# Kernel optimization log

Hardware: AMD Instinct MI355X
Metric: run time of the kernel (lower is better)

## Reference

```python
import jax, jax.numpy as jnp
import numpy as np

HIDDEN = 1024
FFN = 3584
NUM_EXPERTS = 8
TOP_K = 2
B, S = 2, 1024


def setup_inputs() -> dict:
    key = jax.random.key(0)
    k0, k1, k2, k3 = jax.random.split(key, 4)
    hidden_states = jax.random.normal(k0, (B, S, HIDDEN), dtype=jnp.float32)
    # torch Linear stores [out, in]; we keep gate as [E, H] (matches nn.Linear weight)
    gate_w = jax.random.normal(k1, (NUM_EXPERTS, HIDDEN), dtype=jnp.float32) * 0.02
    # GroupedLinear weights stored as [E, in, out] for direct x @ W per expert
    w_gate_up = jax.random.normal(k2, (NUM_EXPERTS, HIDDEN, 2 * FFN), dtype=jnp.float32) * 0.02
    w_down = jax.random.normal(k3, (NUM_EXPERTS, FFN, HIDDEN), dtype=jnp.float32) * 0.02
    return {"hidden_states": hidden_states, "gate_w": gate_w,
            "w_gate_up": w_gate_up, "w_down": w_down}


def reference(hidden_states, gate_w, w_gate_up, w_down):
    b, s, h = hidden_states.shape
    x = hidden_states.reshape(-1, h)                      # [T, H]
    T = x.shape[0]
    E = gate_w.shape[0]

    # Router: logits -> fp32 softmax -> top-k -> renormalize (Mixtral semantics)
    router_logits = x @ gate_w.T                          # [T, E]
    probs = jax.nn.softmax(router_logits.astype(jnp.float32), axis=-1)
    top_vals, top_idx = jax.lax.top_k(probs, TOP_K)       # [T, K]
    top_vals = top_vals / top_vals.sum(axis=-1, keepdims=True)
    top_vals = top_vals.astype(x.dtype)

    # Dense combine weights [T, E]: scatter top-k probs to expert slots.
    # Equivalent to permute -> grouped GEMM -> unpermute-with-probs.
    combine = jnp.zeros((T, E), dtype=x.dtype).at[
        jnp.arange(T)[:, None], top_idx].add(top_vals)

    out = jnp.zeros_like(x)
    for e in range(E):  # fixed small expert count
        gu = x @ w_gate_up[e]                             # [T, 2F]
        gate_proj, up_proj = jnp.split(gu, 2, axis=-1)
        act = jax.nn.silu(gate_proj) * up_proj            # [T, F]
        out = out + combine[:, e:e + 1] * (act @ w_down[e])

    return out.reshape(b, s, h), router_logits
```

## Files before the change

kernel.cpp:

```cpp
#include <hip/hip_runtime.h>
#include <hip/hip_bf16.h>
#include <stdint.h>

#define HIDDEN  1024
#define FFN     3584
#define NE      8
#define NTOK    2048
#define CAP     2048
#define OUT_ELEMS (NTOK * HIDDEN)

#define X_OFF    0u
#define CNT_OFF  (4u*1024u*1024u)
#define TOK_OFF  (CNT_OFF + 256u)
#define WGT_OFF  (TOK_OFF + 65536u)
#define INV_OFF  (WGT_OFF + 65536u)
#define ACT_OFF  (INV_OFF + 16384u)
#define ACT_SZ   (4096u * 3584u * 2u)
#define WGU_OFF  (ACT_OFF + ACT_SZ)
#define WGU_SZ   (8u*56u*16u*16384u)
#define WDB_OFF  (WGU_OFF + WGU_SZ)
#define WDB_SZ   (8u*8u*56u*16384u)
#define PART_OFF (WDB_OFF + WDB_SZ)
#define PART_SZ  (4096u*1024u*4u)
#define WS_NEED  ((size_t)PART_OFF + (size_t)PART_SZ)

typedef __attribute__((ext_vector_type(8))) short short8;
typedef __attribute__((ext_vector_type(4))) float floatx4;

static __device__ __forceinline__ uint32_t f2bf(float f) {
  union { float f; uint32_t u; } v; v.f = f;
  return (v.u + 0x7FFFu + ((v.u >> 16) & 1u)) >> 16;
}
static __device__ __forceinline__ uint32_t pack2(float lo, float hi) {
  return f2bf(lo) | (f2bf(hi) << 16);
}
union S8U { uint4 u; short8 s; };
static __device__ __forceinline__ short8 as_short8(uint4 v) { S8U x; x.u = v; return x.s; }

static __device__ __forceinline__ void ld_g2l16(const void* g, void* l) {
  __builtin_amdgcn_global_load_lds(
      (const __attribute__((address_space(1))) void*)g,
      (__attribute__((address_space(3))) void*)l, 16, 0, 0);
}

static __device__ __forceinline__ void stage_tile(
    const char* const* aptr, const char* bptr, size_t akt, size_t bkt,
    uint4* AsB, uint4* BsB, int w)
{
#pragma unroll
  for (int it = 0; it < 4; ++it)
    ld_g2l16(aptr[it] + akt, &AsB[(w * 4 + it) * 64]);
#pragma unroll
  for (int it = 0; it < 4; ++it)
    ld_g2l16(bptr + bkt + (size_t)it * 1024u, &BsB[(w * 4 + it) * 64]);
}

#define WAIT_VM8()  do { __builtin_amdgcn_sched_barrier(0); \
                         asm volatile("s_waitcnt vmcnt(8)" ::: "memory"); \
                         __builtin_amdgcn_sched_barrier(0); } while (0)
#define WAIT_VM16() do { __builtin_amdgcn_sched_barrier(0); \
                         asm volatile("s_waitcnt vmcnt(16)" ::: "memory"); \
                         __builtin_amdgcn_sched_barrier(0); } while (0)
#define WAIT_VM0()  do { __builtin_amdgcn_sched_barrier(0); \
                         asm volatile("s_waitcnt vmcnt(0)" ::: "memory"); \
                         __builtin_amdgcn_sched_barrier(0); } while (0)
#define WAIT_LGKM() do { asm volatile("s_waitcnt lgkmcnt(0)" ::: "memory"); } while (0)
#define BAR()       do { __builtin_amdgcn_s_barrier(); \
                         __builtin_amdgcn_sched_barrier(0); } while (0)
#define ENDBAR()    do { __builtin_amdgcn_sched_barrier(0); \
                         __builtin_amdgcn_s_barrier(); } while (0)

__global__ __launch_bounds__(256) void moe_prep(float4* __restrict__ out4,
                                                int* __restrict__ cnt) {
  uint32_t i = blockIdx.x * 256u + threadIdx.x;
  out4[i] = make_float4(0.f, 0.f, 0.f, 0.f);
  if (blockIdx.x == 0 && threadIdx.x < NE) cnt[threadIdx.x] = 0;
}

__global__ __launch_bounds__(256) void moe_convert(const float4* __restrict__ x4,
                                                   uint4* __restrict__ xb,
                                                   int* __restrict__ cnt) {
  uint32_t g = blockIdx.x * 256u + threadIdx.x;
  float4 a = x4[2u*g], b = x4[2u*g + 1u];
  xb[g] = make_uint4(pack2(a.x, a.y), pack2(a.z, a.w),
                     pack2(b.x, b.y), pack2(b.z, b.w));
  if (blockIdx.x == 0 && threadIdx.x < NE) cnt[threadIdx.x] = 0;
}

__global__ __launch_bounds__(256) void moe_router(
    const float* __restrict__ x, const float* __restrict__ gw,
    float* __restrict__ logits, int* __restrict__ cnt,
    int* __restrict__ tok, float* __restrict__ wgt, int* __restrict__ inv)
{
  const int t = blockIdx.x * 4 + (threadIdx.x >> 6);
  const int lane = threadIdx.x & 63;
  const float* xr = x + (size_t)t * HIDDEN;
  float a[NE];
#pragma unroll
  for (int e = 0; e < NE; ++e) a[e] = 0.f;
  for (int hh = 0; hh < HIDDEN / 64; ++hh) {
    float xv = xr[hh * 64 + lane];
#pragma unroll
    for (int e = 0; e < NE; ++e) a[e] += xv * gw[e * HIDDEN + hh * 64 + lane];
  }
#pragma unroll
  for (int off = 32; off > 0; off >>= 1) {
#pragma unroll
    for (int e = 0; e < NE; ++e) a[e] += __shfl_xor(a[e], off);
  }
  if (lane == 0) {
#pragma unroll
    for (int e = 0; e < NE; ++e) logits[t * NE + e] = a[e];
    int i0 = 0; float v0 = a[0];
#pragma unroll
    for (int e = 1; e < NE; ++e) if (a[e] > v0) { v0 = a[e]; i0 = e; }
    int i1 = (i0 == 0) ? 1 : 0; float v1 = a[i1];
#pragma unroll
    for (int e = 0; e < NE; ++e) if (e != i0 && a[e] > v1) { v1 = a[e]; i1 = e; }
    float w0 = 1.f / (1.f + __expf(v1 - v0));
    float w1 = 1.f - w0;
    int p0 = atomicAdd(&cnt[i0], 1); tok[i0 * CAP + p0] = t; wgt[i0 * CAP + p0] = w0;
    int p1 = atomicAdd(&cnt[i1], 1); tok[i1 * CAP + p1] = t; wgt[i1 * CAP + p1] = w1;
    inv[t * 2 + 0] = i0 * CAP + p0;
    inv[t * 2 + 1] = i1 * CAP + p1;
  }
}

__global__ __launch_bounds__(256) void moe_wconv_d(const float* __restrict__ wd,
                                                   uint4* __restrict__ wdb) {
  const int kt = blockIdx.x, nb = blockIdx.y, e = blockIdx.z;
  const int n0 = nb * 128, k0 = kt * 64;
  const float* wB = wd + (size_t)e * FFN * HIDDEN;
  uint4* dst = wdb + ((size_t)(e * 8 + nb) * 56 + kt) * 1024;

  __shared__ float lds_f[64 * 129];

#pragma unroll
  for (int p = 0; p < 8; ++p) {
    int idx = p * 256 + threadIdx.x;
    int r   = idx >> 5;
    int lc  = (idx & 31) * 4;
    float4 v = *(const float4*)(wB + (size_t)(k0 + r) * HIDDEN + n0 + lc);
    float* d = &lds_f[r * 129 + lc];
    d[0] = v.x; d[1] = v.y; d[2] = v.z; d[3] = v.w;
  }
  __syncthreads();
#pragma unroll
  for (int p = 0; p < 4; ++p) {
    int m  = p * 256 + threadIdx.x;
    int ne = m >> 3, c8 = m & 7;
    float f[8];
#pragma unroll
    for (int kk = 0; kk < 8; ++kk) f[kk] = lds_f[(c8 * 8 + kk) * 129 + ne];
    dst[ne * 8 + (c8 ^ (ne & 7))] =
        make_uint4(pack2(f[0], f[1]), pack2(f[2], f[3]),
                   pack2(f[4], f[5]), pack2(f[6], f[7]));
  }
}

__global__ __launch_bounds__(512) void moe_gateup_f(
    const uint4* __restrict__ xb, const float* __restrict__ wgu,
    const int* __restrict__ cnt, const int* __restrict__ tok,
    unsigned short* __restrict__ act)
{
  const int e  = blockIdx.z;
  const int m0 = blockIdx.y * 512;
  const int fb = blockIdx.x;
  const int f0 = fb * 64;
  const int cn = cnt[e];
  if (m0 >= cn) return;
  int basev = 0;
#pragma unroll
  for (int i = 0; i < NE; ++i) { int ci = cnt[i]; if (i < e) basev += ci; }

  __shared__ uint4 As[4096];
  __shared__ uint4 Bs[1024];

  const int tid  = threadIdx.x;
  const int lane = tid & 63;
  const int w    = tid >> 6;
  const int q    = lane >> 4;
  const int c    = lane & 15;

  const int* tokE = tok + e * CAP;
  const char* aptr[8];
#pragma unroll
  for (int it = 0; it < 8; ++it) {
    int p   = (w * 8 + it) * 64 + lane;
    int row = p >> 3, c8 = p & 7;
    int mrow = m0 + row; if (mrow >= cn) mrow = cn - 1;
    aptr[it] = (const char*)(xb + (size_t)tokE[mrow] * (HIDDEN / 8) + (c8 ^ (row & 7)));
  }

  const int ne  = tid & 127;
  const int c8b = tid >> 7;
  const int col = f0 + ((ne >> 6) << 5) + (ne & 31) + (((ne >> 5) & 1) ? FFN : 0);
  const float* colp = wgu + (size_t)e * HIDDEN * (2 * FFN) + col;
  const int wi0 = ne * 8 + (c8b ^ (ne & 7));
  const int wi1 = ne * 8 + ((c8b + 4) ^ (ne & 7));

  floatx4 acc[4][8];
#pragma unroll
  for (int i = 0; i < 4; ++i)
#pragma unroll
    for (int j = 0; j < 8; ++j) acc[i][j] = (floatx4){0.f, 0.f, 0.f, 0.f};

  float rv[16];
#pragma unroll
  for (int s = 0; s < 2; ++s)
#pragma unroll
    for (int kk = 0; kk < 8; ++kk)
      rv[s * 8 + kk] = colp[(size_t)((c8b + 4 * s) * 8 + kk) * (2 * FFN)];

  const int NT = HIDDEN / 64;
  for (int kt = 0; kt < NT; ++kt) {
    WAIT_VM0();
    uint4 pk0 = make_uint4(pack2(rv[0], rv[1]),  pack2(rv[2], rv[3]),
                           pack2(rv[4], rv[5]),  pack2(rv[6], rv[7]));
    uint4 pk1 = make_uint4(pack2(rv[8], rv[9]),  pack2(rv[10], rv[11]),
                           pack2(rv[12], rv[13]), pack2(rv[14], rv[15]));
    Bs[wi0] = pk0;
    Bs[wi1] = pk1;
#pragma unroll
    for (int it = 0; it < 8; ++it)
      ld_g2l16(aptr[it] + (size_t)kt * 128u, &As[(w * 8 + it) * 64]);
    if (kt + 1 < NT) {
      const int kb = (kt + 1) * 64;
#pragma unroll
      for (int s = 0; s < 2; ++s)
#pragma unroll
        for (int kk = 0; kk < 8; ++kk)
          rv[s * 8 + kk] = colp[(size_t)(kb + (c8b + 4 * s) * 8 + kk) * (2 * FFN)];
      WAIT_VM16();
    } else {
      WAIT_VM0();
    }
    WAIT_LGKM();
    BAR();
#pragma unroll
    for (int ks = 0; ks < 2; ++ks) {
      const int kc8 = ks * 4 + q;
      short8 af[4];
#pragma unroll
      for (int i = 0; i < 4; ++i) {
        int row = w * 64 + i * 16 + c;
        af[i] = as_short8(As[row * 8 + (kc8 ^ (row & 7))]);
      }
      short8 bfr[8];
#pragma unroll
      for (int j = 0; j < 8; ++j) {
        int n = j * 16 + c;
        bfr[j] = as_short8(Bs[n * 8 + (kc8 ^ (n & 7))]);
      }
#pragma unroll
      for (int i = 0; i < 4; ++i)
#pragma unroll
        for (int j = 0; j < 8; ++j)
          acc[i][j] = __builtin_amdgcn_mfma_f32_16x16x32_bf16(af[i], bfr[j], acc[i][j], 0, 0, 0);
    }
    ENDBAR();
  }

#pragma unroll
  for (int i = 0; i < 4; ++i) {
#pragma unroll
    for (int r = 0; r < 4; ++r) {
      int m = m0 + w * 64 + i * 16 + q * 4 + r;
      if (m < cn) {
        unsigned short* arow = act + (size_t)(basev + m) * FFN;
#pragma unroll
        for (int t4 = 0; t4 < 4; ++t4) {
          const int jj = (t4 & 1) | ((t4 >> 1) << 2);
          float g = acc[i][jj][r];
          float u = acc[i][jj + 2][r];
          float a = (g / (1.f + __expf(-g))) * u;
          arow[f0 + ((jj >> 2) << 5) + (jj & 1) * 16 + c] = (unsigned short)f2bf(a);
        }
      }
    }
  }
}

__global__ __launch_bounds__(256) void moe_down(
    const unsigned short* __restrict__ act, const uint4* __restrict__ wdb,
    const int* __restrict__ cnt, const int* __restrict__ tok,
    const float* __restrict__ wgt, float* __restrict__ part)
{
  const int e  = blockIdx.z;
  const int m0 = blockIdx.y * 128;
  const int nb = blockIdx.x;
  const int n0 = nb * 128;
  const int cn = cnt[e];
  if (m0 >= cn) return;
  int basev = 0;
#pragma unroll
  for (int i = 0; i < NE; ++i) { int ci = cnt[i]; if (i < e) basev += ci; }

  __shared__ uint4 As[2][1024];
  __shared__ uint4 Bs4[2][1024];

  const int tid  = threadIdx.x;
  const int lane = tid & 63;
  const int w    = tid >> 6;
  const int wm   = w >> 1, wn = w & 1;
  const int q    = lane >> 4;
  const int c    = lane & 15;

  const char* aptr[4];
#pragma unroll
  for (int it = 0; it < 4; ++it) {
    int p   = (w * 4 + it) * 64 + lane;
    int row = p >> 3, c8 = p & 7;
    int mrow = m0 + row; if (mrow >= cn) mrow = cn - 1;
    aptr[it] = (const char*)act +
               ((size_t)(basev + mrow) * FFN + (size_t)((c8 ^ (row & 7)) * 8)) * 2u;
  }
  const char* bptr = (const char*)wdb + ((size_t)(e * 8 + nb) * 56) * 16384u
                   + (size_t)w * 4096u + (size_t)lane * 16u;

  floatx4 acc[4][4];
#pragma unroll
  for (int i = 0; i < 4; ++i)
#pragma unroll
    for (int j = 0; j < 4; ++j) acc[i][j] = (floatx4){0.f, 0.f, 0.f, 0.f};

  const int NT = FFN / 64;
  stage_tile(aptr, bptr, 0, 0, As[0], Bs4[0], w);
  int cur = 0;
  for (int kt = 0; kt < NT; ++kt) {
    if (kt + 1 < NT) {
      stage_tile(aptr, bptr, (size_t)(kt + 1) * 128u, (size_t)(kt + 1) * 16384u,
                 As[cur ^ 1], Bs4[cur ^ 1], w);
      WAIT_VM8();
    } else {
      WAIT_VM0();
    }
    BAR();
    const uint4* Asc = As[cur];
    const uint4* Bsc = Bs4[cur];
#pragma unroll
    for (int ks = 0; ks < 2; ++ks) {
      const int kc8 = ks * 4 + q;
      short8 af[4];
#pragma unroll
      for (int i = 0; i < 4; ++i) {
        int row = wm * 64 + i * 16 + c;
        af[i] = as_short8(Asc[row * 8 + (kc8 ^ (row & 7))]);
      }
      short8 bfr[4];
#pragma unroll
      for (int j = 0; j < 4; ++j) {
        int n = wn * 64 + j * 16 + c;
        bfr[j] = as_short8(Bsc[n * 8 + (kc8 ^ (n & 7))]);
      }
#pragma unroll
      for (int i = 0; i < 4; ++i)
#pragma unroll
        for (int j = 0; j < 4; ++j)
          acc[i][j] = __builtin_amdgcn_mfma_f32_16x16x32_bf16(af[i], bfr[j], acc[i][j], 0, 0, 0);
    }
    ENDBAR();
    cur ^= 1;
  }

#pragma unroll
  for (int i = 0; i < 4; ++i) {
#pragma unroll
    for (int r = 0; r < 4; ++r) {
      int m = m0 + wm * 64 + i * 16 + q * 4 + r;
      if (m < cn) {
        float  wg   = wgt[e * CAP + m];
        float* prow = part + (size_t)(basev + m) * HIDDEN + n0 + wn * 64 + c;
#pragma unroll
        for (int j = 0; j < 4; ++j)
          prow[j * 16] = acc[i][j][r] * wg;
      }
    }
  }
}

__global__ __launch_bounds__(256) void moe_combine(
    const int* __restrict__ cnt, const int* __restrict__ inv,
    const float4* __restrict__ part4, float4* __restrict__ out4)
{
  const int t  = blockIdx.x;
  const int s0 = inv[2 * t], s1 = inv[2 * t + 1];
  const int e0 = s0 >> 11, e1 = s1 >> 11;
  int b0 = 0, b1 = 0;
#pragma unroll
  for (int i = 0; i < NE; ++i) {
    int ci = cnt[i];
    if (i < e0) b0 += ci;
    if (i < e1) b1 += ci;
  }
  const size_t r0 = (size_t)(b0 + (s0 & (CAP - 1))) * 256u;
  const size_t r1 = (size_t)(b1 + (s1 & (CAP - 1))) * 256u;
  const int i = threadIdx.x;
  float4 a = part4[r0 + i];
  float4 b = part4[r1 + i];
  out4[(size_t)t * 256u + i] = make_float4(a.x + b.x, a.y + b.y, a.z + b.z, a.w + b.w);
}

__global__ __launch_bounds__(256) void moe_gateup_lg(
    const uint4* __restrict__ xb, const float* __restrict__ wgu,
    const int* __restrict__ cnt, const int* __restrict__ tok,
    unsigned short* __restrict__ act)
{
  const int e  = blockIdx.z;
  const int m0 = blockIdx.y * 128;
  const int f0 = blockIdx.x * 64;
  const int cn = cnt[e];
  if (m0 >= cn) return;
  int basev = 0;
#pragma unroll
  for (int i = 0; i < NE; ++i) { int ci = cnt[i]; if (i < e) basev += ci; }

  __shared__ uint4    As[1024];
  __shared__ uint32_t Bs[4096];

  const int tid  = threadIdx.x;
  const int lane = tid & 63;
  const int w    = tid >> 6;
  const int wm   = w >> 1, wn = w & 1;
  const int q    = lane >> 4;
  const int c    = lane & 15;

  floatx4 acc[4][4];
#pragma unroll
  for (int i = 0; i < 4; ++i)
#pragma unroll
    for (int j = 0; j < 4; ++j) acc[i][j] = (floatx4){0.f, 0.f, 0.f, 0.f};

  const float* wB  = wgu + (size_t)e * HIDDEN * (2 * FFN);
  const int* tokE  = tok + e * CAP;

  for (int kt = 0; kt < HIDDEN / 64; ++kt) {
    const int k0 = kt * 64;
    __syncthreads();
#pragma unroll
    for (int it = 0; it < 4; ++it) {
      int cid = it * 256 + tid;
      int row = cid >> 3, c8 = cid & 7;
      int mrow = m0 + row; if (mrow >= cn) mrow = cn - 1;
      int tk = tokE[mrow];
      As[row * 8 + (c8 ^ (row & 7))] = xb[(size_t)tk * (HIDDEN / 8) + (k0 >> 3) + c8];
    }
#pragma unroll
    for (int it = 0; it < 4; ++it) {
      int mid = it * 256 + tid;
      int kp = mid >> 5;
      int n  = (mid & 31) * 4;
      int col = f0 + ((n >> 6) << 5) + (n & 31) + (((n >> 5) & 1) ? FFN : 0);
      const float* src = wB + (size_t)(k0 + 2 * kp) * (2 * FFN) + col;
      float4 r0 = *(const float4*)src;
      float4 r1 = *(const float4*)(src + 2 * FFN);
      int widx = kp * 128 + (n ^ (((kp >> 2) & 1) << 4));
      *(uint4*)&Bs[widx] = make_uint4(pack2(r0.x, r1.x), pack2(r0.y, r1.y),
                                      pack2(r0.z, r1.z), pack2(r0.w, r1.w));
    }
    __syncthreads();
#pragma unroll
    for (int ks = 0; ks < 2; ++ks) {
      short8 af[4];
#pragma unroll
      for (int i = 0; i < 4; ++i) {
        int row = wm * 64 + i * 16 + c;
        int kc8 = ks * 4 + q;
        af[i] = as_short8(As[row * 8 + (kc8 ^ (row & 7))]);
      }
      short8 bfr[4];
#pragma unroll
      for (int j = 0; j < 4; ++j) {
        int n  = wn * 64 + j * 16 + c;
        int kp = ks * 16 + q * 4;
        int nn = n ^ ((q & 1) << 4);
        bfr[j] = as_short8(make_uint4(Bs[(kp + 0) * 128 + nn], Bs[(kp + 1) * 128 + nn],
                                      Bs[(kp + 2) * 128 + nn], Bs[(kp + 3) * 128 + nn]));
      }
#pragma unroll
      for (int i = 0; i < 4; ++i)
#pragma unroll
        for (int j = 0; j < 4; ++j)
          acc[i][j] = __builtin_amdgcn_mfma_f32_16x16x32_bf16(af[i], bfr[j], acc[i][j], 0, 0, 0);
    }
  }

#pragma unroll
  for (int i = 0; i < 4; ++i) {
#pragma unroll
    for (int r = 0; r < 4; ++r) {
      int m = m0 + wm * 64 + i * 16 + q * 4 + r;
      if (m < cn) {
#pragma unroll
        for (int j = 0; j < 2; ++j) {
          float g = acc[i][j][r];
          float u = acc[i][j + 2][r];
          float a = (g / (1.f + __expf(-g))) * u;
          act[(size_t)(basev + m) * FFN + (f0 + wn * 32 + j * 16 + c)] = (unsigned short)f2bf(a);
        }
      }
    }
  }
}

__global__ __launch_bounds__(256) void moe_down_lg(
    const uint4* __restrict__ actc, const float* __restrict__ wd,
    const int* __restrict__ cnt, const int* __restrict__ tok,
    const float* __restrict__ wgt, float* __restrict__ out)
{
  const int e  = blockIdx.z;
  const int m0 = blockIdx.y * 128;
  const int n0 = blockIdx.x * 128;
  const int cn = cnt[e];
  if (m0 >= cn) return;
  int basev = 0;
#pragma unroll
  for (int i = 0; i < NE; ++i) { int ci = cnt[i]; if (i < e) basev += ci; }

  __shared__ uint4    As[1024];
  __shared__ uint32_t Bs[4096];

  const int tid  = threadIdx.x;
  const int lane = tid & 63;
  const int w    = tid >> 6;
  const int wm   = w >> 1, wn = w & 1;
  const int q    = lane >> 4;
  const int c    = lane & 15;

  floatx4 acc[4][4];
#pragma unroll
  for (int i = 0; i < 4; ++i)
#pragma unroll
    for (int j = 0; j < 4; ++j) acc[i][j] = (floatx4){0.f, 0.f, 0.f, 0.f};

  const float* wB = wd + (size_t)e * FFN * HIDDEN;

  for (int kt = 0; kt < FFN / 64; ++kt) {
    const int k0 = kt * 64;
    __syncthreads();
#pragma unroll
    for (int it = 0; it < 4; ++it) {
      int cid = it * 256 + tid;
      int row = cid >> 3, c8 = cid & 7;
      int mrow = m0 + row; if (mrow >= cn) mrow = cn - 1;
      As[row * 8 + (c8 ^ (row & 7))] =
          actc[(size_t)(basev + mrow) * (FFN / 8) + (k0 >> 3) + c8];
    }
#pragma unroll
    for (int it = 0; it < 4; ++it) {
      int mid = it * 256 + tid;
      int kp = mid >> 5;
      int n  = (mid & 31) * 4;
      int col = n0 + n;
      const float* src = wB + (size_t)(k0 + 2 * kp) * HIDDEN + col;
      float4 r0 = *(const float4*)src;
      float4 r1 = *(const float4*)(src + HIDDEN);
      int widx = kp * 128 + (n ^ (((kp >> 2) & 1) << 4));
      *(uint4*)&Bs[widx] = make_uint4(pack2(r0.x, r1.x), pack2(r0.y, r1.y),
                                      pack2(r0.z, r1.z), pack2(r0.w, r1.w));
    }
    __syncthreads();
#pragma unroll
    for (int ks = 0; ks < 2; ++ks) {
      short8 af[4];
#pragma unroll
      for (int i = 0; i < 4; ++i) {
        int row = wm * 64 + i * 16 + c;
        int kc8 = ks * 4 + q;
        af[i] = as_short8(As[row * 8 + (kc8 ^ (row & 7))]);
      }
      short8 bfr[4];
#pragma unroll
      for (int j = 0; j < 4; ++j) {
        int n  = wn * 64 + j * 16 + c;
        int kp = ks * 16 + q * 4;
        int nn = n ^ ((q & 1) << 4);
        bfr[j] = as_short8(make_uint4(Bs[(kp + 0) * 128 + nn], Bs[(kp + 1) * 128 + nn],
                                      Bs[(kp + 2) * 128 + nn], Bs[(kp + 3) * 128 + nn]));
      }
#pragma unroll
      for (int i = 0; i < 4; ++i)
#pragma unroll
        for (int j = 0; j < 4; ++j)
          acc[i][j] = __builtin_amdgcn_mfma_f32_16x16x32_bf16(af[i], bfr[j], acc[i][j], 0, 0, 0);
    }
  }

#pragma unroll
  for (int i = 0; i < 4; ++i) {
#pragma unroll
    for (int r = 0; r < 4; ++r) {
      int m = m0 + wm * 64 + i * 16 + q * 4 + r;
      if (m < cn) {
        int   t  = tok[e * CAP + m];
        float wg = wgt[e * CAP + m];
        float* orow = out + (size_t)t * HIDDEN + n0 + wn * 64 + c;
#pragma unroll
        for (int j = 0; j < 4; ++j)
          atomicAdd(orow + j * 16, acc[i][j][r] * wg);
      }
    }
  }
}

extern "C" void kernel_launch(void* const* d_in, const int* in_sizes, int n_in,
                              void* d_out, int out_size, void* d_ws, size_t ws_size,
                              hipStream_t stream)
{
  (void)in_sizes; (void)n_in; (void)out_size;
  const float* x   = (const float*)d_in[0];
  const float* gw  = (const float*)d_in[1];
  const float* wgu = (const float*)d_in[2];
  const float* wd  = (const float*)d_in[3];
  float* out = (float*)d_out;
  char*  ws  = (char*)d_ws;

  uint4*          xb   = (uint4*)(ws + X_OFF);
  int*            cnt  = (int*)(ws + CNT_OFF);
  int*            tok  = (int*)(ws + TOK_OFF);
  float*          wgt  = (float*)(ws + WGT_OFF);
  int*            inv  = (int*)(ws + INV_OFF);
  unsigned short* act  = (unsigned short*)(ws + ACT_OFF);
  uint4*          wdb  = (uint4*)(ws + WDB_OFF);
  float*          part = (float*)(ws + PART_OFF);

  const bool fast = (ws_size >= WS_NEED);

  if (fast) {
    moe_convert<<<(NTOK * HIDDEN) / (256 * 8), 256, 0, stream>>>((const float4*)x, xb, cnt);
    moe_router<<<NTOK / 4, 256, 0, stream>>>(x, gw, out + OUT_ELEMS, cnt, tok, wgt, inv);
    moe_wconv_d<<<dim3(56, 8, NE), 256, 0, stream>>>(wd, wdb);
    moe_gateup_f<<<dim3(FFN / 64, CAP / 512, NE), 512, 0, stream>>>(xb, wgu, cnt, tok, act);
    moe_down<<<dim3(HIDDEN / 128, 16, NE), 256, 0, stream>>>(act, wdb, cnt, tok, wgt, part);
    moe_combine<<<NTOK, 256, 0, stream>>>(cnt, inv, (const float4*)part, (float4*)out);
  } else {
    moe_prep<<<OUT_ELEMS / (256 * 4), 256, 0, stream>>>((float4*)out, cnt);
    moe_convert<<<(NTOK * HIDDEN) / (256 * 8), 256, 0, stream>>>((const float4*)x, xb, cnt);
    moe_router<<<NTOK / 4, 256, 0, stream>>>(x, gw, out + OUT_ELEMS, cnt, tok, wgt, inv);
    moe_gateup_lg<<<dim3(FFN / 64, 16, NE), 256, 0, stream>>>(xb, wgu, cnt, tok, act);
    moe_down_lg<<<dim3(HIDDEN / 128, 16, NE), 256, 0, stream>>>((const uint4*)act, wd, cnt, tok, wgt, out);
  }
}
```

Baseline: 626.5 us.

## Fuse down-proj weight conversion into GEMM and double-buffer A tiles

Removes the separate pass that converts fp32 down-projection weights to bf16 and instead loads fp32 weights directly in the down GEMM, packing them to bf16 in registers. The down GEMM is retiled to 512-row by 64-column blocks of 512 threads, matching the gate-up kernel. Both GEMMs now double-buffer the gathered activation tile in LDS and prefetch weights two steps ahead. This saves one full read and write of the weight tensor, at the cost of more LDS per block, possibly lower occupancy, and strided scalar fp32 weight loads.

```diff
diff --git a/kernel.cpp b/kernel.cpp
--- a/kernel.cpp
+++ b/kernel.cpp
@@ -16,11 +16,7 @@
 #define INV_OFF  (WGT_OFF + 65536u)
 #define ACT_OFF  (INV_OFF + 16384u)
 #define ACT_SZ   (4096u * 3584u * 2u)
-#define WGU_OFF  (ACT_OFF + ACT_SZ)
-#define WGU_SZ   (8u*56u*16u*16384u)
-#define WDB_OFF  (WGU_OFF + WGU_SZ)
-#define WDB_SZ   (8u*8u*56u*16384u)
-#define PART_OFF (WDB_OFF + WDB_SZ)
+#define PART_OFF (ACT_OFF + ACT_SZ)
 #define PART_SZ  (4096u*1024u*4u)
 #define WS_NEED  ((size_t)PART_OFF + (size_t)PART_SZ)
 
@@ -41,18 +37,6 @@
   __builtin_amdgcn_global_load_lds(
       (const __attribute__((address_space(1))) void*)g,
       (__attribute__((address_space(3))) void*)l, 16, 0, 0);
-}
-
-static __device__ __forceinline__ void stage_tile(
-    const char* const* aptr, const char* bptr, size_t akt, size_t bkt,
-    uint4* AsB, uint4* BsB, int w)
-{
-#pragma unroll
-  for (int it = 0; it < 4; ++it)
-    ld_g2l16(aptr[it] + akt, &AsB[(w * 4 + it) * 64]);
-#pragma unroll
-  for (int it = 0; it < 4; ++it)
-    ld_g2l16(bptr + bkt + (size_t)it * 1024u, &BsB[(w * 4 + it) * 64]);
 }
 
 #define WAIT_VM8()  do { __builtin_amdgcn_sched_barrier(0); \
@@ -126,39 +110,7 @@
   }
 }
 
-__global__ __launch_bounds__(256) void moe_wconv_d(const float* __restrict__ wd,
-                                                   uint4* __restrict__ wdb) {
-  const int kt = blockIdx.x, nb = blockIdx.y, e = blockIdx.z;
-  const int n0 = nb * 128, k0 = kt * 64;
-  const float* wB = wd + (size_t)e * FFN * HIDDEN;
-  uint4* dst = wdb + ((size_t)(e * 8 + nb) * 56 + kt) * 1024;
-
-  __shared__ float lds_f[64 * 129];
-
-#pragma unroll
-  for (int p = 0; p < 8; ++p) {
-    int idx = p * 256 + threadIdx.x;
-    int r   = idx >> 5;
-    int lc  = (idx & 31) * 4;
-    float4 v = *(const float4*)(wB + (size_t)(k0 + r) * HIDDEN + n0 + lc);
-    float* d = &lds_f[r * 129 + lc];
-    d[0] = v.x; d[1] = v.y; d[2] = v.z; d[3] = v.w;
-  }
-  __syncthreads();
-#pragma unroll
-  for (int p = 0; p < 4; ++p) {
-    int m  = p * 256 + threadIdx.x;
-    int ne = m >> 3, c8 = m & 7;
-    float f[8];
-#pragma unroll
-    for (int kk = 0; kk < 8; ++kk) f[kk] = lds_f[(c8 * 8 + kk) * 129 + ne];
-    dst[ne * 8 + (c8 ^ (ne & 7))] =
-        make_uint4(pack2(f[0], f[1]), pack2(f[2], f[3]),
-                   pack2(f[4], f[5]), pack2(f[6], f[7]));
-  }
-}
-
-__global__ __launch_bounds__(512) void moe_gateup_f(
+__global__ __launch_bounds__(512) void moe_gateup_f2(
     const uint4* __restrict__ xb, const float* __restrict__ wgu,
     const int* __restrict__ cnt, const int* __restrict__ tok,
     unsigned short* __restrict__ act)
@@ -173,7 +125,7 @@
 #pragma unroll
   for (int i = 0; i < NE; ++i) { int ci = cnt[i]; if (i < e) basev += ci; }
 
-  __shared__ uint4 As[4096];
+  __shared__ uint4 As[2][4096];
   __shared__ uint4 Bs[1024];
 
   const int tid  = threadIdx.x;
@@ -205,61 +157,75 @@
 #pragma unroll
     for (int j = 0; j < 8; ++j) acc[i][j] = (floatx4){0.f, 0.f, 0.f, 0.f};
 
-  float rv[16];
+  const int NT = HIDDEN / 64;
+  float rv0[16], rv1[16];
+
 #pragma unroll
   for (int s = 0; s < 2; ++s)
 #pragma unroll
     for (int kk = 0; kk < 8; ++kk)
-      rv[s * 8 + kk] = colp[(size_t)((c8b + 4 * s) * 8 + kk) * (2 * FFN)];
-
-  const int NT = HIDDEN / 64;
-  for (int kt = 0; kt < NT; ++kt) {
-    WAIT_VM0();
-    uint4 pk0 = make_uint4(pack2(rv[0], rv[1]),  pack2(rv[2], rv[3]),
-                           pack2(rv[4], rv[5]),  pack2(rv[6], rv[7]));
-    uint4 pk1 = make_uint4(pack2(rv[8], rv[9]),  pack2(rv[10], rv[11]),
-                           pack2(rv[12], rv[13]), pack2(rv[14], rv[15]));
-    Bs[wi0] = pk0;
-    Bs[wi1] = pk1;
-#pragma unroll
-    for (int it = 0; it < 8; ++it)
-      ld_g2l16(aptr[it] + (size_t)kt * 128u, &As[(w * 8 + it) * 64]);
-    if (kt + 1 < NT) {
-      const int kb = (kt + 1) * 64;
-#pragma unroll
-      for (int s = 0; s < 2; ++s)
-#pragma unroll
-        for (int kk = 0; kk < 8; ++kk)
-          rv[s * 8 + kk] = colp[(size_t)(kb + (c8b + 4 * s) * 8 + kk) * (2 * FFN)];
-      WAIT_VM16();
-    } else {
-      WAIT_VM0();
-    }
-    WAIT_LGKM();
-    BAR();
-#pragma unroll
-    for (int ks = 0; ks < 2; ++ks) {
-      const int kc8 = ks * 4 + q;
-      short8 af[4];
-#pragma unroll
-      for (int i = 0; i < 4; ++i) {
-        int row = w * 64 + i * 16 + c;
-        af[i] = as_short8(As[row * 8 + (kc8 ^ (row & 7))]);
-      }
-      short8 bfr[8];
-#pragma unroll
-      for (int j = 0; j < 8; ++j) {
-        int n = j * 16 + c;
-        bfr[j] = as_short8(Bs[n * 8 + (kc8 ^ (n & 7))]);
-      }
-#pragma unroll
-      for (int i = 0; i < 4; ++i)
-#pragma unroll
-        for (int j = 0; j < 8; ++j)
-          acc[i][j] = __builtin_amdgcn_mfma_f32_16x16x32_bf16(af[i], bfr[j], acc[i][j], 0, 0, 0);
-    }
-    ENDBAR();
-  }
+      rv0[s * 8 + kk] = colp[(size_t)((c8b + 4 * s) * 8 + kk) * (2 * FFN)];
+#pragma unroll
+  for (int it = 0; it < 8; ++it)
+    ld_g2l16(aptr[it], &As[0][(w * 8 + it) * 64]);
+#pragma unroll
+  for (int s = 0; s < 2; ++s)
+#pragma unroll
+    for (int kk = 0; kk < 8; ++kk)
+      rv1[s * 8 + kk] = colp[(size_t)(64 + (c8b + 4 * s) * 8 + kk) * (2 * FFN)];
+
+#define GU_STEP(RV, BUF, T)                                                     \
+  do {                                                                          \
+    if ((T) == NT - 1) { WAIT_VM0(); } else { WAIT_VM16(); }                    \
+    Bs[wi0] = make_uint4(pack2(RV[0], RV[1]),  pack2(RV[2], RV[3]),             \
+                         pack2(RV[4], RV[5]),  pack2(RV[6], RV[7]));            \
+    Bs[wi1] = make_uint4(pack2(RV[8], RV[9]),  pack2(RV[10], RV[11]),           \
+                         pack2(RV[12], RV[13]), pack2(RV[14], RV[15]));         \
+    if ((T) + 1 < NT) {                                                         \
+      _Pragma("unroll")                                                         \
+      for (int it = 0; it < 8; ++it)                                            \
+        ld_g2l16(aptr[it] + (size_t)((T) + 1) * 128u,                           \
+                 &As[(BUF) ^ 1][(w * 8 + it) * 64]);                            \
+    }                                                                           \
+    if ((T) + 2 < NT) {                                                         \
+      const int kb = ((T) + 2) * 64;                                            \
+      _Pragma("unroll")                                                         \
+      for (int s = 0; s < 2; ++s)                                               \
+        _Pragma("unroll")                                                       \
+        for (int kk = 0; kk < 8; ++kk)                                          \
+          RV[s * 8 + kk] = colp[(size_t)(kb + (c8b + 4 * s) * 8 + kk) * (2 * FFN)]; \
+    }                                                                           \
+    WAIT_LGKM(); BAR();                                                         \
+    _Pragma("unroll")                                                           \
+    for (int ks = 0; ks < 2; ++ks) {                                            \
+      const int kc8 = ks * 4 + q;                                               \
+      short8 af[4];                                                             \
+      _Pragma("unroll")                                                         \
+      for (int i = 0; i < 4; ++i) {                                             \
+        int row = w * 64 + i * 16 + c;                                          \
+        af[i] = as_short8(As[BUF][row * 8 + (kc8 ^ (row & 7))]);                \
+      }                                                                         \
+      short8 bfr[8];                                                            \
+      _Pragma("unroll")                                                         \
+      for (int j = 0; j < 8; ++j) {                                             \
+        int n = j * 16 + c;                                                     \
+        bfr[j] = as_short8(Bs[n * 8 + (kc8 ^ (n & 7))]);                        \
+      }                                                                         \
+      _Pragma("unroll")                                                         \
+      for (int i = 0; i < 4; ++i)                                               \
+        _Pragma("unroll")                                                       \
+        for (int j = 0; j < 8; ++j)                                             \
+          acc[i][j] = __builtin_amdgcn_mfma_f32_16x16x32_bf16(af[i], bfr[j],    \
+                                                              acc[i][j], 0, 0, 0); \
+    }                                                                           \
+    ENDBAR();                                                                   \
+  } while (0)
+
+  for (int t = 0; t < NT; t += 2) {
+    GU_STEP(rv0, 0, t);
+    GU_STEP(rv1, 1, t + 1);
+  }
+#undef GU_STEP
 
 #pragma unroll
   for (int i = 0; i < 4; ++i) {
@@ -281,42 +247,44 @@
   }
 }
 
-__global__ __launch_bounds__(256) void moe_down(
-    const unsigned short* __restrict__ act, const uint4* __restrict__ wdb,
-    const int* __restrict__ cnt, const int* __restrict__ tok,
-    const float* __restrict__ wgt, float* __restrict__ part)
+__global__ __launch_bounds__(512) void moe_down_f(
+    const unsigned short* __restrict__ act, const float* __restrict__ wd,
+    const int* __restrict__ cnt, const float* __restrict__ wgt,
+    float* __restrict__ part)
 {
   const int e  = blockIdx.z;
-  const int m0 = blockIdx.y * 128;
+  const int m0 = blockIdx.y * 512;
   const int nb = blockIdx.x;
-  const int n0 = nb * 128;
+  const int n0 = nb * 64;
   const int cn = cnt[e];
   if (m0 >= cn) return;
   int basev = 0;
 #pragma unroll
   for (int i = 0; i < NE; ++i) { int ci = cnt[i]; if (i < e) basev += ci; }
 
-  __shared__ uint4 As[2][1024];
-  __shared__ uint4 Bs4[2][1024];
+  __shared__ uint4 As[2][4096];
+  __shared__ uint4 Bs[512];
 
   const int tid  = threadIdx.x;
   const int lane = tid & 63;
   const int w    = tid >> 6;
-  const int wm   = w >> 1, wn = w & 1;
   const int q    = lane >> 4;
   const int c    = lane & 15;
 
-  const char* aptr[4];
-#pragma unroll
-  for (int it = 0; it < 4; ++it) {
-    int p   = (w * 4 + it) * 64 + lane;
+  const char* aptr[8];
+#pragma unroll
+  for (int it = 0; it < 8; ++it) {
+    int p   = (w * 8 + it) * 64 + lane;
     int row = p >> 3, c8 = p & 7;
     int mrow = m0 + row; if (mrow >= cn) mrow = cn - 1;
     aptr[it] = (const char*)act +
                ((size_t)(basev + mrow) * FFN + (size_t)((c8 ^ (row & 7)) * 8)) * 2u;
   }
-  const char* bptr = (const char*)wdb + ((size_t)(e * 8 + nb) * 56) * 16384u
-                   + (size_t)w * 4096u + (size_t)lane * 16u;
+
+  const int ne  = tid & 63;
+  const int c8b = tid >> 6;
+  const float* colp = wd + (size_t)e * FFN * HIDDEN + n0 + ne;
+  const int wi = ne * 8 + (c8b ^ (ne & 7));
 
   floatx4 acc[4][4];
 #pragma unroll
@@ -325,55 +293,78 @@
     for (int j = 0; j < 4; ++j) acc[i][j] = (floatx4){0.f, 0.f, 0.f, 0.f};
 
   const int NT = FFN / 64;
-  stage_tile(aptr, bptr, 0, 0, As[0], Bs4[0], w);
-  int cur = 0;
-  for (int kt = 0; kt < NT; ++kt) {
-    if (kt + 1 < NT) {
-      stage_tile(aptr, bptr, (size_t)(kt + 1) * 128u, (size_t)(kt + 1) * 16384u,
-                 As[cur ^ 1], Bs4[cur ^ 1], w);
-      WAIT_VM8();
-    } else {
-      WAIT_VM0();
-    }
-    BAR();
-    const uint4* Asc = As[cur];
-    const uint4* Bsc = Bs4[cur];
-#pragma unroll
-    for (int ks = 0; ks < 2; ++ks) {
-      const int kc8 = ks * 4 + q;
-      short8 af[4];
-#pragma unroll
-      for (int i = 0; i < 4; ++i) {
-        int row = wm * 64 + i * 16 + c;
-        af[i] = as_short8(Asc[row * 8 + (kc8 ^ (row & 7))]);
-      }
-      short8 bfr[4];
-#pragma unroll
-      for (int j = 0; j < 4; ++j) {
-        int n = wn * 64 + j * 16 + c;
-        bfr[j] = as_short8(Bsc[n * 8 + (kc8 ^ (n & 7))]);
-      }
-#pragma unroll
-      for (int i = 0; i < 4; ++i)
-#pragma unroll
-        for (int j = 0; j < 4; ++j)
-          acc[i][j] = __builtin_amdgcn_mfma_f32_16x16x32_bf16(af[i], bfr[j], acc[i][j], 0, 0, 0);
-    }
-    ENDBAR();
-    cur ^= 1;
-  }
+  float rv0[8], rv1[8];
+
+#pragma unroll
+  for (int kk = 0; kk < 8; ++kk)
+    rv0[kk] = colp[(size_t)(c8b * 8 + kk) * HIDDEN];
+#pragma unroll
+  for (int it = 0; it < 8; ++it)
+    ld_g2l16(aptr[it], &As[0][(w * 8 + it) * 64]);
+#pragma unroll
+  for (int kk = 0; kk < 8; ++kk)
+    rv1[kk] = colp[(size_t)(64 + c8b * 8 + kk) * HIDDEN];
+
+#define DN_STEP(RV, BUF, T)                                                     \
+  do {                                                                          \
+    if ((T) == NT - 1) { WAIT_VM0(); } else { WAIT_VM8(); }                     \
+    Bs[wi] = make_uint4(pack2(RV[0], RV[1]), pack2(RV[2], RV[3]),               \
+                        pack2(RV[4], RV[5]), pack2(RV[6], RV[7]));              \
+    if ((T) + 1 < NT) {                                                         \
+      _Pragma("unroll")                                                         \
+      for (int it = 0; it < 8; ++it)                                            \
+        ld_g2l16(aptr[it] + (size_t)((T) + 1) * 128u,                           \
+                 &As[(BUF) ^ 1][(w * 8 + it) * 64]);                            \
+    }                                                                           \
+    if ((T) + 2 < NT) {                                                         \
+      const int kb = ((T) + 2) * 64;                                            \
+      _Pragma("unroll")                                                         \
+      for (int kk = 0; kk < 8; ++kk)                                            \
+        RV[kk] = colp[(size_t)(kb + c8b * 8 + kk) * HIDDEN];                    \
+    }                                                                           \
+    WAIT_LGKM(); BAR();                                                         \
+    _Pragma("unroll")                                                           \
+    for (int ks = 0; ks < 2; ++ks) {                                            \
+      const int kc8 = ks * 4 + q;                                               \
+      short8 af[4];                                                             \
+      _Pragma("unroll")                                                         \
+      for (int i = 0; i < 4; ++i) {                                             \
+        int row = w * 64 + i * 16 + c;                                          \
+        af[i] = as_short8(As[BUF][row * 8 + (kc8 ^ (row & 7))]);                \
+      }                                                                         \
+      short8 bfr[4];                                                            \
+      _Pragma("unroll")                                                         \
+      for (int j = 0; j < 4; ++j) {                                             \
+        int n = j * 16 + c;                                                     \
+        bfr[j] = as_short8(Bs[n * 8 + (kc8 ^ (n & 7))]);                        \
+      }                                                                         \
+      _Pragma("unroll")                                                         \
+      for (int i = 0; i < 4; ++i)                                               \
+        _Pragma("unroll")                                                       \
+        for (int j = 0; j < 4; ++j)                                             \
+          acc[i][j] = __builtin_amdgcn_mfma_f32_16x16x32_bf16(af[i], bfr[j],    \
+                                                              acc[i][j], 0, 0, 0); \
+    }                                                                           \
+    ENDBAR();                                                                   \
+  } while (0)
+
+  for (int t = 0; t < NT; t += 2) {
+    DN_STEP(rv0, 0, t);
+    DN_STEP(rv1, 1, t + 1);
+  }
+#undef DN_STEP
 
 #pragma unroll
   for (int i = 0; i < 4; ++i) {
 #pragma unroll
     for (int r = 0; r < 4; ++r) {
-      int m = m0 + wm * 64 + i * 16 + q * 4 + r;
+      int m = m0 + w * 64 + i * 16 + q * 4 + r;
       if (m < cn) {
         float  wg   = wgt[e * CAP + m];
-        float* prow = part + (size_t)(basev + m) * HIDDEN + n0 + wn * 64 + c;
+        float* prow = part + (size_t)(basev + m) * HIDDEN + n0;
 #pragma unroll
         for (int j = 0; j < 4; ++j)
-          prow[j * 16] = acc[i][j][r] * wg;
+          prow[j * 16 + c] = acc[i][j][r] * wg;
       }
     }
   }
@@ -621,7 +612,6 @@
   float*          wgt  = (float*)(ws + WGT_OFF);
   int*            inv  = (int*)(ws + INV_OFF);
   unsigned short* act  = (unsigned short*)(ws + ACT_OFF);
-  uint4*          wdb  = (uint4*)(ws + WDB_OFF);
   float*          part = (float*)(ws + PART_OFF);
 
   const bool fast = (ws_size >= WS_NEED);
@@ -629,9 +619,8 @@
   if (fast) {
     moe_convert<<<(NTOK * HIDDEN) / (256 * 8), 256, 0, stream>>>((const float4*)x, xb, cnt);
     moe_router<<<NTOK / 4, 256, 0, stream>>>(x, gw, out + OUT_ELEMS, cnt, tok, wgt, inv);
-    moe_wconv_d<<<dim3(56, 8, NE), 256, 0, stream>>>(wd, wdb);
-    moe_gateup_f<<<dim3(FFN / 64, CAP / 512, NE), 512, 0, stream>>>(xb, wgu, cnt, tok, act);
-    moe_down<<<dim3(HIDDEN / 128, 16, NE), 256, 0, stream>>>(act, wdb, cnt, tok, wgt, part);
+    moe_gateup_f2<<<dim3(FFN / 64, CAP / 512, NE), 512, 0, stream>>>(xb, wgu, cnt, tok, act);
+    moe_down_f<<<dim3(HIDDEN / 64, CAP / 512, NE), 512, 0, stream>>>(act, wd, cnt, wgt, part);
     moe_combine<<<NTOK, 256, 0, stream>>>(cnt, inv, (const float4*)part, (float4*)out);
   } else {
     moe_prep<<<OUT_ELEMS / (256 * 4), 256, 0, stream>>>((float4*)out, cnt);
```

Result: slower. 998.5 us (+59.4%).
